# Optimization experiments

Measured on AMD Instinct MI355X. Metric: run time of the kernel, lower is better.

The kernel has to match this reference:

```python
import jax, jax.numpy as jnp
import numpy as np

FP16_HUGE = 2.0 ** 15
NUM_HEAD = 4
LN_EPS = 1e-5


def setup_inputs() -> dict:
    key = jax.random.key(0)
    ks = jax.random.split(key, 12)
    B, N, D = 1, 256, 128
    H = NUM_HEAD
    inp = {
        "pair_act": jax.random.normal(ks[0], (B, N, N, D), dtype=jnp.float32),
        "pair_mask": jnp.ones((B, N, N), dtype=jnp.float32),
        "ln_scale": jnp.ones((D,), dtype=jnp.float32),
        "ln_bias": jnp.zeros((D,), dtype=jnp.float32),
        # torch Linear weight layout: [out_dim, in_dim]; applied as x @ W.T
        "w2d": jax.random.normal(ks[1], (H, D), dtype=jnp.float32) / np.sqrt(D),
        "wq": jax.random.normal(ks[2], (D, D), dtype=jnp.float32) / np.sqrt(D),
        "wk": jax.random.normal(ks[3], (D, D), dtype=jnp.float32) / np.sqrt(D),
        "wv": jax.random.normal(ks[4], (D, D), dtype=jnp.float32) / np.sqrt(D),
        "wg": jax.random.normal(ks[5], (D, D), dtype=jnp.float32) / np.sqrt(D),
        "bg": jnp.ones((D,), dtype=jnp.float32),  # gating bias init = 1.0
        "wo": jax.random.normal(ks[6], (D, D), dtype=jnp.float32) * 0.02,
        "bo": jnp.zeros((D,), dtype=jnp.float32),
    }
    return inp


def reference(pair_act, pair_mask, ln_scale, ln_bias, w2d, wq, wk, wv, wg, bg, wo, bo):
    B, N, _, D = pair_act.shape
    H = NUM_HEAD
    kd = D // H  # per-head key/value dim
    scale = kd ** (-0.5)

    # mask bias: [B, N(row), 1, 1, N(key)]
    bias = (FP16_HUGE * (pair_mask - 1.0))[:, :, None, None, :]

    # LayerNorm (fp32, eps=1e-5)
    mu = jnp.mean(pair_act, axis=-1, keepdims=True)
    var = jnp.mean(jnp.square(pair_act - mu), axis=-1, keepdims=True)
    x = (pair_act - mu) * jax.lax.rsqrt(var + LN_EPS) * ln_scale + ln_bias

    # non-batched per-head bias: [B, 1, H, N, N]
    nb = jnp.einsum("bijd,hd->bhij", x, w2d)[:, None]

    q = (x @ wq.T).reshape(B, N, N, H, kd) * scale  # [B, r, i, H, kd]
    k = (x @ wk.T).reshape(B, N, N, H, kd)
    v = (x @ wv.T).reshape(B, N, N, H, kd)

    logits = jnp.einsum("brihk,brjhk->brhij", q, k) + bias + nb  # [B, r, H, i, j]
    w = jax.nn.softmax(logits, axis=-1)
    o = jnp.einsum("brhij,brjhv->brihv", w, v)  # [B, r, i, H, kd]

    g = jax.nn.sigmoid(x @ wg.T + bg).reshape(B, N, N, H, kd)
    o = (o * g).reshape(B, N, N, D)

    out = o @ wo.T + bo
    return out * pair_mask[..., None]
```

## Files before the change

### kernel.cpp

```cpp
#include <hip/hip_runtime.h>
#include <hip/hip_bf16.h>

typedef unsigned short u16;
typedef __attribute__((ext_vector_type(8))) short bf16x8;
typedef __attribute__((ext_vector_type(4))) float f32x4;
typedef __attribute__((address_space(3))) unsigned lds_u32;
typedef const __attribute__((address_space(1))) unsigned glb_u32;

#define N 256
#define D 128
#define NH 4
#define KD 32
#define NN 65536
#define QK_SCALE 0.17677669529663687f
#define LOG2E 1.4426950408889634f
#define HUGE_MASK 32768.0f

__device__ __forceinline__ float b2f(u16 s) {
  union { float f; unsigned u; } x; x.u = ((unsigned)s) << 16; return x.f;
}
__device__ __forceinline__ u16 f2b(float f) {
  union { float f; unsigned u; } x; x.f = f;
  unsigned r = x.u + 0x7fff + ((x.u >> 16) & 1);
  return (u16)(r >> 16);
}

__global__ __launch_bounds__(256) void prep_w_kernel(
    const float* __restrict__ wq, const float* __restrict__ wk,
    const float* __restrict__ wv, const float* __restrict__ wg,
    const float* __restrict__ wo, u16* __restrict__ wb)
{
  int idx = blockIdx.x * 256 + threadIdx.x;
  const float* srcs[5] = {wq, wk, wv, wg, wo};
  int mat = idx >> 11, rem = idx & 2047;
  int row = rem >> 4, g = rem & 15;
  int gp = (g + (row & 15)) & 15;
  const float* s = srcs[mat] + row * 128 + g * 8;
  float4 f0 = *(const float4*)(s);
  float4 f1 = *(const float4*)(s + 4);
  uint4 pk;
  pk.x = (unsigned)f2b(f0.x) | ((unsigned)f2b(f0.y) << 16);
  pk.y = (unsigned)f2b(f0.z) | ((unsigned)f2b(f0.w) << 16);
  pk.z = (unsigned)f2b(f1.x) | ((unsigned)f2b(f1.y) << 16);
  pk.w = (unsigned)f2b(f1.z) | ((unsigned)f2b(f1.w) << 16);
  *(uint4*)(wb + (size_t)mat * 16384 + row * 128 + gp * 8) = pk;
}

__device__ __forceinline__ void async_stage(const u16* __restrict__ gsrc, u16* lds, int tid) {
  int lane = tid & 63, wave = tid >> 6;
  u16* lbase = lds + wave * 512;
  const u16* gbase = gsrc + wave * 512 + lane * 8;
#pragma unroll
  for (int p = 0; p < 8; p++) {
    __builtin_amdgcn_global_load_lds((glb_u32*)(gbase + p * 2048),
                                     (lds_u32*)(lbase + p * 2048), 16, 0, 0);
  }
}

__global__ __launch_bounds__(256) void projln_kernel(
    const float* __restrict__ pa, const float* __restrict__ lns, const float* __restrict__ lnb,
    const float* __restrict__ w2d, const u16* __restrict__ wb, const float* __restrict__ bg,
    u16* __restrict__ q, u16* __restrict__ k, u16* __restrict__ v, u16* __restrict__ g,
    float* __restrict__ nb)
{
  __shared__ __align__(16) u16 Wl[2][16384];
  int tid = threadIdx.x;
  int wave = tid >> 6, lane = tid & 63;
  int lr = lane & 15, quad = lane >> 4;

  async_stage(wb, Wl[0], tid);

  bf16x8 a[2][4];
#pragma unroll
  for (int mt = 0; mt < 2; mt++) {
    int row = blockIdx.x * 128 + wave * 32 + mt * 16 + lr;
    const float* rp = pa + (size_t)row * D;
    float xv[4][8];
    float s = 0.f, ss = 0.f;
#pragma unroll
    for (int ks = 0; ks < 4; ks++) {
      float4 a0 = *(const float4*)(rp + ks * 32 + quad * 8);
      float4 a1 = *(const float4*)(rp + ks * 32 + quad * 8 + 4);
      xv[ks][0] = a0.x; xv[ks][1] = a0.y; xv[ks][2] = a0.z; xv[ks][3] = a0.w;
      xv[ks][4] = a1.x; xv[ks][5] = a1.y; xv[ks][6] = a1.z; xv[ks][7] = a1.w;
#pragma unroll
      for (int j = 0; j < 8; j++) { s += xv[ks][j]; ss += xv[ks][j] * xv[ks][j]; }
    }
    s  += __shfl_xor(s, 16, 64);  ss += __shfl_xor(ss, 16, 64);
    s  += __shfl_xor(s, 32, 64);  ss += __shfl_xor(ss, 32, 64);
    float mu = s * (1.0f / D);
    float var = ss * (1.0f / D) - mu * mu;
    float rs = rsqrtf(var + 1e-5f);
#pragma unroll
    for (int ks = 0; ks < 4; ks++) {
      float4 s0 = *(const float4*)(lns + ks * 32 + quad * 8);
      float4 s1 = *(const float4*)(lns + ks * 32 + quad * 8 + 4);
      float4 b0 = *(const float4*)(lnb + ks * 32 + quad * 8);
      float4 b1 = *(const float4*)(lnb + ks * 32 + quad * 8 + 4);
      float sc[8] = {s0.x,s0.y,s0.z,s0.w,s1.x,s1.y,s1.z,s1.w};
      float bi[8] = {b0.x,b0.y,b0.z,b0.w,b1.x,b1.y,b1.z,b1.w};
#pragma unroll
      for (int j = 0; j < 8; j++) xv[ks][j] = (xv[ks][j] - mu) * rs * sc[j] + bi[j];
    }
#pragma unroll
    for (int h = 0; h < NH; h++) {
      float p = 0.f;
#pragma unroll
      for (int ks = 0; ks < 4; ks++) {
        float4 w0 = *(const float4*)(w2d + h * D + ks * 32 + quad * 8);
        float4 w1 = *(const float4*)(w2d + h * D + ks * 32 + quad * 8 + 4);
        p += xv[ks][0]*w0.x + xv[ks][1]*w0.y + xv[ks][2]*w0.z + xv[ks][3]*w0.w
           + xv[ks][4]*w1.x + xv[ks][5]*w1.y + xv[ks][6]*w1.z + xv[ks][7]*w1.w;
      }
      p += __shfl_xor(p, 16, 64);
      p += __shfl_xor(p, 32, 64);
      if (quad == 0) nb[(size_t)h * NN + row] = p * LOG2E;
    }
#pragma unroll
    for (int ks = 0; ks < 4; ks++)
#pragma unroll
      for (int j = 0; j < 8; j++) a[mt][ks][j] = (short)f2b(xv[ks][j]);
  }
  __syncthreads();

  u16* Os[4] = {q, k, v, g};
#pragma unroll
  for (int mat = 0; mat < 4; mat++) {
    if (mat < 3) async_stage(wb + (size_t)(mat + 1) * 16384, Wl[(mat + 1) & 1], tid);
    const u16* Wcur = Wl[mat & 1];
    f32x4 acc[2][2][4];
#pragma unroll
    for (int mt = 0; mt < 2; mt++)
#pragma unroll
      for (int tg = 0; tg < 2; tg++)
#pragma unroll
        for (int e = 0; e < 4; e++) acc[mt][tg][e] = (f32x4){0.f, 0.f, 0.f, 0.f};
#pragma unroll
    for (int ks = 0; ks < 4; ks++) {
#pragma unroll
      for (int tg = 0; tg < 2; tg++) {
#pragma unroll
        for (int e = 0; e < 4; e++) {
          int nrow = tg * 64 + 4 * lr + e;
          int gp = (ks * 4 + quad + (nrow & 15)) & 15;
          bf16x8 b = *(const bf16x8*)(&Wcur[nrow * 128 + gp * 8]);
          acc[0][tg][e] = __builtin_amdgcn_mfma_f32_16x16x32_bf16(a[0][ks], b, acc[0][tg][e], 0, 0, 0);
          acc[1][tg][e] = __builtin_amdgcn_mfma_f32_16x16x32_bf16(a[1][ks], b, acc[1][tg][e], 0, 0, 0);
        }
      }
    }
    u16* O = Os[mat];
#pragma unroll
    for (int mt = 0; mt < 2; mt++) {
      int row0 = blockIdx.x * 128 + wave * 32 + mt * 16 + quad * 4;
#pragma unroll
      for (int tg = 0; tg < 2; tg++) {
        int c0 = tg * 64 + 4 * lr;
        float bg0 = 0.f, bg1 = 0.f, bg2 = 0.f, bg3 = 0.f;
        if (mat == 3) { bg0 = bg[c0]; bg1 = bg[c0+1]; bg2 = bg[c0+2]; bg3 = bg[c0+3]; }
#pragma unroll
        for (int reg = 0; reg < 4; reg++) {
          float v0 = acc[mt][tg][0][reg], v1 = acc[mt][tg][1][reg];
          float v2 = acc[mt][tg][2][reg], v3 = acc[mt][tg][3][reg];
          if (mat == 0) {
            v0 *= QK_SCALE * LOG2E; v1 *= QK_SCALE * LOG2E;
            v2 *= QK_SCALE * LOG2E; v3 *= QK_SCALE * LOG2E;
          }
          if (mat == 3) {
            v0 = 1.0f / (1.0f + __expf(-(v0 + bg0)));
            v1 = 1.0f / (1.0f + __expf(-(v1 + bg1)));
            v2 = 1.0f / (1.0f + __expf(-(v2 + bg2)));
            v3 = 1.0f / (1.0f + __expf(-(v3 + bg3)));
          }
          uint2 pk;
          pk.x = (unsigned)f2b(v0) | ((unsigned)f2b(v1) << 16);
          pk.y = (unsigned)f2b(v2) | ((unsigned)f2b(v3) << 16);
          *(uint2*)(O + (size_t)(row0 + reg) * D + c0) = pk;
        }
      }
    }
    __syncthreads();
  }
}

__global__ __launch_bounds__(256, 2) void attn_kernel(
    const u16* __restrict__ q, const u16* __restrict__ k, const u16* __restrict__ v,
    const u16* __restrict__ g, const float* __restrict__ nb, const float* __restrict__ mask,
    u16* __restrict__ og)
{
  __shared__ __align__(16) u16 Kf[8192];
  __shared__ __align__(16) u16 Vf[8192];
  __shared__ __align__(16) u16 Pf[16384];
  __shared__ float bias_lds[256];
  int h = blockIdx.x & 3, r = blockIdx.x >> 2;
  int tid = threadIdx.x;
  {
    int j = tid;
    const u16* krow = k + ((size_t)r * N + j) * D + h * KD;
    int t = j >> 4, lrj = j & 15;
#pragma unroll
    for (int qc = 0; qc < 4; qc++)
      *(bf16x8*)(&Kf[((t * 4 + qc) * 16 + lrj) * 8]) = *(const bf16x8*)(krow + qc * 8);
    const u16* vrow = v + ((size_t)r * N + j) * D + h * KD;
    int ks = j >> 5, qj = (j >> 3) & 3, jj = j & 7;
#pragma unroll
    for (int cc = 0; cc < 32; cc++) {
      int c = (cc + qj * 8) & 31;
      Vf[(((ks * 2 + (c & 1)) * 4 + qj) * 16 + (c >> 1)) * 8 + jj] = vrow[c];
    }
    bias_lds[tid] = (HUGE_MASK * LOG2E) * (mask[r * N + tid] - 1.0f);
  }
  __syncthreads();
  int wave = tid >> 6, lane = tid & 63;
  int lr = lane & 15, quad = lane >> 4;
  u16* Pw = &Pf[wave * 4096];

  bf16x8 af[4], gv[4];
#pragma unroll
  for (int pass = 0; pass < 4; pass++) {
    int i0 = pass * 64 + wave * 16;
    size_t base = ((size_t)r * N + i0 + lr) * D + h * KD + quad * 8;
    af[pass] = *(const bf16x8*)(q + base);
    gv[pass] = *(const bf16x8*)(g + base);
  }

  for (int pass = 0; pass < 4; pass++) {
    int i0 = pass * 64 + wave * 16;
    const float* nbrow = nb + (size_t)h * NN + (size_t)(i0 + lr) * N;
    float4 nbv[16];
#pragma unroll
    for (int t = 0; t < 16; t++) nbv[t] = *(const float4*)(nbrow + t * 16 + quad * 4);
    f32x4 S[16];
#pragma unroll
    for (int t = 0; t < 16; t++) {
      bf16x8 kf = *(const bf16x8*)(&Kf[((t * 4 + quad) * 16 + lr) * 8]);
      S[t] = __builtin_amdgcn_mfma_f32_16x16x32_bf16(kf, af[pass], (f32x4){0.f,0.f,0.f,0.f}, 0, 0, 0);
    }
    float lsum = 0.f;
#pragma unroll
    for (int t = 0; t < 16; t++) {
      float4 b4 = *(const float4*)(&bias_lds[t * 16 + quad * 4]);
      float e0 = exp2f(S[t][0] + nbv[t].x + b4.x);
      float e1 = exp2f(S[t][1] + nbv[t].y + b4.y);
      float e2 = exp2f(S[t][2] + nbv[t].z + b4.z);
      float e3 = exp2f(S[t][3] + nbv[t].w + b4.w);
      lsum += (e0 + e1) + (e2 + e3);
      union { float f; unsigned u; } c0, c1, c2, c3;
      c0.f = e0; c1.f = e1; c2.f = e2; c3.f = e3;
      uint2 pk;
      pk.x = ((c0.u + 0x8000u) >> 16) | ((c1.u + 0x8000u) & 0xffff0000u);
      pk.y = ((c2.u + 0x8000u) >> 16) | ((c3.u + 0x8000u) & 0xffff0000u);
      int ks = t >> 1;
      int qc = 2 * (t & 1) + (quad >> 1);
      *(uint2*)(&Pw[((ks * 4 + qc) * 16 + lr) * 8 + 4 * (quad & 1)]) = pk;
    }
    lsum += __shfl_xor(lsum, 16, 64);
    lsum += __shfl_xor(lsum, 32, 64);
    float inv = __builtin_amdgcn_rcpf(lsum);
    __asm__ __volatile__("s_waitcnt lgkmcnt(0)" ::: "memory");
    f32x4 o[2] = {(f32x4){0.f,0.f,0.f,0.f}, (f32x4){0.f,0.f,0.f,0.f}};
#pragma unroll
    for (int ks = 0; ks < 8; ks++) {
      bf16x8 pb = *(const bf16x8*)(&Pw[((ks * 4 + quad) * 16 + lr) * 8]);
#pragma unroll
      for (int e = 0; e < 2; e++) {
        bf16x8 vb = *(const bf16x8*)(&Vf[(((ks * 2 + e) * 4 + quad) * 16 + lr) * 8]);
        o[e] = __builtin_amdgcn_mfma_f32_16x16x32_bf16(vb, pb, o[e], 0, 0, 0);
      }
    }
    size_t base = ((size_t)r * N + i0 + lr) * D + h * KD + quad * 8;
    bf16x8 pk8;
#pragma unroll
    for (int reg = 0; reg < 4; reg++) {
#pragma unroll
      for (int e = 0; e < 2; e++) {
        float val = o[e][reg] * inv * b2f((u16)gv[pass][2 * reg + e]);
        pk8[2 * reg + e] = (short)f2b(val);
      }
    }
    *(bf16x8*)(og + base) = pk8;
  }
}

__global__ __launch_bounds__(256) void out_kernel(
    const u16* __restrict__ og, const u16* __restrict__ wob, const float* __restrict__ bo,
    const float* __restrict__ mask, float* __restrict__ out)
{
  __shared__ __align__(16) u16 Wlds[16384];
  int tid = threadIdx.x;
  async_stage(wob, Wlds, tid);
  int wave = tid >> 6, lane = tid & 63;
  int lr = lane & 15, quad = lane >> 4;
  bf16x8 a[2][4];
#pragma unroll
  for (int mt = 0; mt < 2; mt++) {
    int arow = blockIdx.x * 128 + wave * 32 + mt * 16 + lr;
#pragma unroll
    for (int ks = 0; ks < 4; ks++)
      a[mt][ks] = *(const bf16x8*)(og + (size_t)arow * D + ks * 32 + quad * 8);
  }
  __syncthreads();
  f32x4 acc[2][2][4];
#pragma unroll
  for (int mt = 0; mt < 2; mt++)
#pragma unroll
    for (int tg = 0; tg < 2; tg++)
#pragma unroll
      for (int e = 0; e < 4; e++) acc[mt][tg][e] = (f32x4){0.f, 0.f, 0.f, 0.f};
#pragma unroll
  for (int ks = 0; ks < 4; ks++) {
#pragma unroll
    for (int tg = 0; tg < 2; tg++) {
#pragma unroll
      for (int e = 0; e < 4; e++) {
        int nrow = tg * 64 + 4 * lr + e;
        int gp = (ks * 4 + quad + (nrow & 15)) & 15;
        bf16x8 b = *(const bf16x8*)(&Wlds[nrow * 128 + gp * 8]);
        acc[0][tg][e] = __builtin_amdgcn_mfma_f32_16x16x32_bf16(a[0][ks], b, acc[0][tg][e], 0, 0, 0);
        acc[1][tg][e] = __builtin_amdgcn_mfma_f32_16x16x32_bf16(a[1][ks], b, acc[1][tg][e], 0, 0, 0);
      }
    }
  }
#pragma unroll
  for (int mt = 0; mt < 2; mt++) {
    int row0 = blockIdx.x * 128 + wave * 32 + mt * 16 + quad * 4;
#pragma unroll
    for (int tg = 0; tg < 2; tg++) {
      int c0 = tg * 64 + 4 * lr;
      float4 bo4 = *(const float4*)(bo + c0);
#pragma unroll
      for (int reg = 0; reg < 4; reg++) {
        int pos = row0 + reg;
        float m = mask[pos];
        float4 o4;
        o4.x = (acc[mt][tg][0][reg] + bo4.x) * m;
        o4.y = (acc[mt][tg][1][reg] + bo4.y) * m;
        o4.z = (acc[mt][tg][2][reg] + bo4.z) * m;
        o4.w = (acc[mt][tg][3][reg] + bo4.w) * m;
        *(float4*)(out + (size_t)pos * D + c0) = o4;
      }
    }
  }
}

extern "C" void kernel_launch(void* const* d_in, const int* in_sizes, int n_in,
                              void* d_out, int out_size, void* d_ws, size_t ws_size,
                              hipStream_t stream)
{
  const float* pa   = (const float*)d_in[0];
  const float* mask = (const float*)d_in[1];
  const float* lns  = (const float*)d_in[2];
  const float* lnb  = (const float*)d_in[3];
  const float* w2d  = (const float*)d_in[4];
  const float* wq   = (const float*)d_in[5];
  const float* wk   = (const float*)d_in[6];
  const float* wv   = (const float*)d_in[7];
  const float* wg   = (const float*)d_in[8];
  const float* bg   = (const float*)d_in[9];
  const float* wo   = (const float*)d_in[10];
  const float* bo   = (const float*)d_in[11];

  const size_t ARR = (size_t)NN * D;
  u16* q  = (u16*)d_ws;
  u16* k  = q + ARR;
  u16* v  = k + ARR;
  u16* g  = v + ARR;
  u16* og = g + ARR;
  float* nb = (float*)(og + ARR);
  u16* wb = (u16*)(nb + (size_t)NH * NN);

  prep_w_kernel<<<40, 256, 0, stream>>>(wq, wk, wv, wg, wo, wb);
  projln_kernel<<<512, 256, 0, stream>>>(pa, lns, lnb, w2d, wb, bg, q, k, v, g, nb);
  attn_kernel<<<N * NH, 256, 0, stream>>>(q, k, v, g, nb, mask, og);
  out_kernel<<<512, 256, 0, stream>>>(og, wb + 4 * 16384, bo, mask, (float*)d_out);
}
```

Before: 206.9 us.

## Keep softmax probabilities in registers by permuting K layout, drop P LDS buffer

Reorders the K tile layout in LDS so that each lane's QK^T MFMA output lines up with the B-operand layout of the PV MFMA. The exponentiated probabilities can then be packed straight into registers with perm, with no round trip through a per-wave LDS P buffer. Removing the 32KB P buffer lowers LDS use, and launch bounds rise to 4 blocks per CU for more occupancy. The nb bias loads are interleaved into the exp loop, and the q/g prefetch is no longer hoisted, which adds register and latency pressure.

```diff
diff --git a/kernel.cpp b/kernel.cpp
--- a/kernel.cpp
+++ b/kernel.cpp
@@ -183,24 +183,24 @@
   }
 }
 
-__global__ __launch_bounds__(256, 2) void attn_kernel(
+__global__ __launch_bounds__(256, 4) void attn_kernel(
     const u16* __restrict__ q, const u16* __restrict__ k, const u16* __restrict__ v,
     const u16* __restrict__ g, const float* __restrict__ nb, const float* __restrict__ mask,
     u16* __restrict__ og)
 {
   __shared__ __align__(16) u16 Kf[8192];
   __shared__ __align__(16) u16 Vf[8192];
-  __shared__ __align__(16) u16 Pf[16384];
   __shared__ float bias_lds[256];
   int h = blockIdx.x & 3, r = blockIdx.x >> 2;
   int tid = threadIdx.x;
   {
     int j = tid;
+    int tp = 2 * (j >> 5) + ((j >> 2) & 1);
+    int mp = 4 * ((j >> 3) & 3) + (j & 3);
     const u16* krow = k + ((size_t)r * N + j) * D + h * KD;
-    int t = j >> 4, lrj = j & 15;
 #pragma unroll
     for (int qc = 0; qc < 4; qc++)
-      *(bf16x8*)(&Kf[((t * 4 + qc) * 16 + lrj) * 8]) = *(const bf16x8*)(krow + qc * 8);
+      *(bf16x8*)(&Kf[((tp * 4 + qc) * 16 + mp) * 8]) = *(const bf16x8*)(krow + qc * 8);
     const u16* vrow = v + ((size_t)r * N + j) * D + h * KD;
     int ks = j >> 5, qj = (j >> 3) & 3, jj = j & 7;
 #pragma unroll
@@ -213,68 +213,58 @@
   __syncthreads();
   int wave = tid >> 6, lane = tid & 63;
   int lr = lane & 15, quad = lane >> 4;
-  u16* Pw = &Pf[wave * 4096];
-
-  bf16x8 af[4], gv[4];
-#pragma unroll
+
+#pragma unroll 1
   for (int pass = 0; pass < 4; pass++) {
     int i0 = pass * 64 + wave * 16;
     size_t base = ((size_t)r * N + i0 + lr) * D + h * KD + quad * 8;
-    af[pass] = *(const bf16x8*)(q + base);
-    gv[pass] = *(const bf16x8*)(g + base);
-  }
-
-  for (int pass = 0; pass < 4; pass++) {
-    int i0 = pass * 64 + wave * 16;
-    const float* nbrow = nb + (size_t)h * NN + (size_t)(i0 + lr) * N;
-    float4 nbv[16];
-#pragma unroll
-    for (int t = 0; t < 16; t++) nbv[t] = *(const float4*)(nbrow + t * 16 + quad * 4);
+    bf16x8 af = *(const bf16x8*)(q + base);
+    bf16x8 gvv = *(const bf16x8*)(g + base);
     f32x4 S[16];
 #pragma unroll
     for (int t = 0; t < 16; t++) {
       bf16x8 kf = *(const bf16x8*)(&Kf[((t * 4 + quad) * 16 + lr) * 8]);
-      S[t] = __builtin_amdgcn_mfma_f32_16x16x32_bf16(kf, af[pass], (f32x4){0.f,0.f,0.f,0.f}, 0, 0, 0);
-    }
+      S[t] = __builtin_amdgcn_mfma_f32_16x16x32_bf16(kf, af, (f32x4){0.f,0.f,0.f,0.f}, 0, 0, 0);
+    }
+    const float* nbrow = nb + (size_t)h * NN + (size_t)(i0 + lr) * N;
     float lsum = 0.f;
+    uint2 ps[16];
 #pragma unroll
     for (int t = 0; t < 16; t++) {
-      float4 b4 = *(const float4*)(&bias_lds[t * 16 + quad * 4]);
-      float e0 = exp2f(S[t][0] + nbv[t].x + b4.x);
-      float e1 = exp2f(S[t][1] + nbv[t].y + b4.y);
-      float e2 = exp2f(S[t][2] + nbv[t].z + b4.z);
-      float e3 = exp2f(S[t][3] + nbv[t].w + b4.w);
+      int j0 = 32 * (t >> 1) + 8 * quad + 4 * (t & 1);
+      float4 nb4 = *(const float4*)(nbrow + j0);
+      float4 b4 = *(const float4*)(&bias_lds[j0]);
+      float e0 = exp2f(S[t][0] + nb4.x + b4.x);
+      float e1 = exp2f(S[t][1] + nb4.y + b4.y);
+      float e2 = exp2f(S[t][2] + nb4.z + b4.z);
+      float e3 = exp2f(S[t][3] + nb4.w + b4.w);
       lsum += (e0 + e1) + (e2 + e3);
       union { float f; unsigned u; } c0, c1, c2, c3;
       c0.f = e0; c1.f = e1; c2.f = e2; c3.f = e3;
-      uint2 pk;
-      pk.x = ((c0.u + 0x8000u) >> 16) | ((c1.u + 0x8000u) & 0xffff0000u);
-      pk.y = ((c2.u + 0x8000u) >> 16) | ((c3.u + 0x8000u) & 0xffff0000u);
-      int ks = t >> 1;
-      int qc = 2 * (t & 1) + (quad >> 1);
-      *(uint2*)(&Pw[((ks * 4 + qc) * 16 + lr) * 8 + 4 * (quad & 1)]) = pk;
+      ps[t].x = __builtin_amdgcn_perm(c1.u + 0x8000u, c0.u + 0x8000u, 0x07060302u);
+      ps[t].y = __builtin_amdgcn_perm(c3.u + 0x8000u, c2.u + 0x8000u, 0x07060302u);
     }
     lsum += __shfl_xor(lsum, 16, 64);
     lsum += __shfl_xor(lsum, 32, 64);
     float inv = __builtin_amdgcn_rcpf(lsum);
-    __asm__ __volatile__("s_waitcnt lgkmcnt(0)" ::: "memory");
     f32x4 o[2] = {(f32x4){0.f,0.f,0.f,0.f}, (f32x4){0.f,0.f,0.f,0.f}};
 #pragma unroll
     for (int ks = 0; ks < 8; ks++) {
-      bf16x8 pb = *(const bf16x8*)(&Pw[((ks * 4 + quad) * 16 + lr) * 8]);
+      union { uint4 u; bf16x8 b; } pb;
+      pb.u.x = ps[2 * ks].x;     pb.u.y = ps[2 * ks].y;
+      pb.u.z = ps[2 * ks + 1].x; pb.u.w = ps[2 * ks + 1].y;
 #pragma unroll
       for (int e = 0; e < 2; e++) {
         bf16x8 vb = *(const bf16x8*)(&Vf[(((ks * 2 + e) * 4 + quad) * 16 + lr) * 8]);
-        o[e] = __builtin_amdgcn_mfma_f32_16x16x32_bf16(vb, pb, o[e], 0, 0, 0);
-      }
-    }
-    size_t base = ((size_t)r * N + i0 + lr) * D + h * KD + quad * 8;
+        o[e] = __builtin_amdgcn_mfma_f32_16x16x32_bf16(vb, pb.b, o[e], 0, 0, 0);
+      }
+    }
     bf16x8 pk8;
 #pragma unroll
     for (int reg = 0; reg < 4; reg++) {
 #pragma unroll
       for (int e = 0; e < 2; e++) {
-        float val = o[e][reg] * inv * b2f((u16)gv[pass][2 * reg + e]);
+        float val = o[e][reg] * inv * b2f((u16)gvv[2 * reg + e]);
         pk8[2 * reg + e] = (short)f2b(val);
       }
     }
```

After: 309.9 us. 49.8% more time.
